# Kernel optimization log

Hardware: AMD Instinct MI355X
Metric: run time of the kernel (lower is better)

Reference implementation:

```python
import jax, jax.numpy as jnp
import numpy as np

N_LVL = [131072, 32768, 8192, 2048, 512, 256]  # active voxels per pyramid level
B = 8          # point clouds in batch
K = 27         # 3x3x3 kernel offsets
SLOPE = 0.01   # LeakyReLU default negative slope
EPS = 1e-5     # BatchNorm eps


def _bn(x, g, b):
    # MinkowskiBatchNorm, training-mode forward: stats over all points
    m = x.mean(0)
    v = x.var(0)
    return (x - m) * jax.lax.rsqrt(v + EPS) * g + b


def _lrelu(x):
    return jnp.where(x >= 0, x, SLOPE * x)


def _lin_block(x, w, g, b):
    # MinkowskiLinear(bias=False) + BN + LeakyReLU (also models 1x1 conv)
    return _lrelu(_bn(x @ w, g, b))


def _conv_block(x, nbr, w, g, b):
    # sparse conv as gather-GEMM: [N,K,Cin] x [K,Cin,Cout] -> [N,Cout]
    y = jnp.einsum('nkc,kco->no', x[nbr], w)
    return _lrelu(_bn(y, g, b))


def _maxpool(x, pmap):
    # stride-2 kernel-3 sparse max pool via precomputed pooling map
    return x[pmap].max(axis=1)


def setup_inputs() -> dict:
    key = jax.random.key(0)
    ks = iter(jax.random.split(key, 80))

    def nrm(shape, scale):
        return jax.random.normal(next(ks), shape, dtype=jnp.float32) * jnp.float32(scale)

    inp = {}
    inp['x'] = nrm((N_LVL[0], 3), 1.0)
    inp['w_mlp1'] = nrm((3, 16), 1.0 / np.sqrt(3.0))
    inp['g_mlp1'] = jnp.ones(16, jnp.float32)
    inp['b_mlp1'] = jnp.zeros(16, jnp.float32)
    conv_dims = [(16, 32), (32, 48), (48, 96), (96, 128), (128, 256), (256, 512)]
    down_dims = [(48, 32), (80, 48), (144, 96), (224, 128), (384, 256)]
    for i, (ci, co) in enumerate(conv_dims):
        inp[f'w_c{i+1}'] = nrm((K, ci, co), np.sqrt(2.0 / (K * co)))  # kaiming fan_out
        inp[f'g_c{i+1}'] = jnp.ones(co, jnp.float32)
        inp[f'b_c{i+1}'] = jnp.zeros(co, jnp.float32)
    for i, (ci, co) in enumerate(down_dims):
        inp[f'w_d{i+1}'] = nrm((ci, co), np.sqrt(2.0 / co))
        inp[f'g_d{i+1}'] = jnp.ones(co, jnp.float32)
        inp[f'b_d{i+1}'] = jnp.zeros(co, jnp.float32)
    inp['w_f1'] = nrm((1024, 512), 1.0 / 32.0)
    inp['g_f1'] = jnp.ones(512, jnp.float32)
    inp['b_f1'] = jnp.zeros(512, jnp.float32)
    inp['w_f2'] = nrm((512, 256), 1.0 / np.sqrt(512.0))
    inp['g_f2'] = jnp.ones(256, jnp.float32)
    inp['b_f2'] = jnp.zeros(256, jnp.float32)
    inp['w_f3'] = nrm((256, 20), 1.0 / 16.0)
    inp['bias_f3'] = jnp.zeros(20, jnp.float32)
    for i in range(6):
        inp[f'nbr{i}'] = jax.random.randint(next(ks), (N_LVL[i], K), 0, N_LVL[i], dtype=jnp.int32)
    for i in range(1, 6):
        inp[f'pool{i}'] = jax.random.randint(next(ks), (N_LVL[i], K), 0, N_LVL[i - 1], dtype=jnp.int32)
    inp['batch5'] = jnp.repeat(jnp.arange(B, dtype=jnp.int32), N_LVL[5] // B)
    return inp


def reference(x, w_mlp1, g_mlp1, b_mlp1,
              w_c1, g_c1, b_c1, w_c2, g_c2, b_c2, w_c3, g_c3, b_c3,
              w_c4, g_c4, b_c4, w_c5, g_c5, b_c5, w_c6, g_c6, b_c6,
              w_d1, g_d1, b_d1, w_d2, g_d2, b_d2, w_d3, g_d3, b_d3,
              w_d4, g_d4, b_d4, w_d5, g_d5, b_d5,
              w_f1, g_f1, b_f1, w_f2, g_f2, b_f2, w_f3, bias_f3,
              nbr0, nbr1, nbr2, nbr3, nbr4, nbr5,
              pool1, pool2, pool3, pool4, pool5, batch5):
    convs = [(w_c1, g_c1, b_c1), (w_c2, g_c2, b_c2), (w_c3, g_c3, b_c3),
             (w_c4, g_c4, b_c4), (w_c5, g_c5, b_c5)]
    downs = [(w_d1, g_d1, b_d1), (w_d2, g_d2, b_d2), (w_d3, g_d3, b_d3),
             (w_d4, g_d4, b_d4), (w_d5, g_d5, b_d5)]
    nbrs = [nbr0, nbr1, nbr2, nbr3, nbr4]
    pools = [pool1, pool2, pool3, pool4, pool5]

    y = _lin_block(x, w_mlp1, g_mlp1, b_mlp1)  # mlp1, level 0
    for i in range(5):  # fixed 5 conv/cat/down/pool stages (structural loop)
        out = _conv_block(y, nbrs[i], *convs[i])
        y = _lin_block(jnp.concatenate([y, out], axis=1), *downs[i])  # cat + down (1x1)
        y = _maxpool(y, pools[i])
    y = _conv_block(y, nbr5, w_c6, g_c6, b_c6)  # conv6 at level 5: [N5, 512]

    xmax = jax.ops.segment_max(y, batch5, num_segments=B)
    cnt = jax.ops.segment_sum(jnp.ones((y.shape[0], 1), y.dtype), batch5, num_segments=B)
    xavg = jax.ops.segment_sum(y, batch5, num_segments=B) / cnt
    z = jnp.concatenate([xmax, xavg], axis=1)  # [B, 1024]

    z = _lin_block(z, w_f1, g_f1, b_f1)  # dropout = identity (eval)
    z = _lin_block(z, w_f2, g_f2, b_f2)
    return z @ w_f3 + bias_f3  # [B, 20] logits
```

## Files before the change

### kernel.cpp

```cpp
#include <hip/hip_runtime.h>
#include <math.h>

#define BN_EPS 1e-5f


__device__ __forceinline__ void fma4(float s, const float4& w, float4& a) {
    a.x = fmaf(s, w.x, a.x);
    a.y = fmaf(s, w.y, a.y);
    a.z = fmaf(s, w.z, a.z);
    a.w = fmaf(s, w.w, a.w);
}

__device__ __forceinline__ float nlr(float x, float sc, float sh) {
    float t = fmaf(x, sc, sh);
    return fmaxf(t, 0.01f * t);
}

__device__ __forceinline__ void bn_coef(const float* __restrict__ sums,
                                        const float* __restrict__ g,
                                        const float* __restrict__ b,
                                        int C, int c, float inv_n,
                                        float& sc, float& sh) {
    float mean = sums[c] * inv_n;
    float var = fmaxf(fmaf(-mean, mean, sums[C + c] * inv_n), 0.f);
    sc = g[c] * rsqrtf(var + BN_EPS);
    sh = fmaf(-mean, sc, b[c]);
}

__global__ void zero_kernel(float* __restrict__ p, int n) {
    int i = blockIdx.x * blockDim.x + threadIdx.x;
    if (i < n) p[i] = 0.f;
}

__global__ void mlp1_kernel(const float* __restrict__ x, const float* __restrict__ w,
                            float* __restrict__ out, int N) {
    int n = blockIdx.x * blockDim.x + threadIdx.x;
    if (n >= N) return;
    float x0 = x[n * 3], x1 = x[n * 3 + 1], x2 = x[n * 3 + 2];
    #pragma unroll
    for (int c4 = 0; c4 < 4; c4++) {
        float4 w0 = *reinterpret_cast<const float4*>(w + 0 + c4 * 4);
        float4 w1 = *reinterpret_cast<const float4*>(w + 16 + c4 * 4);
        float4 w2 = *reinterpret_cast<const float4*>(w + 32 + c4 * 4);
        float4 o;
        o.x = fmaf(x0, w0.x, fmaf(x1, w1.x, x2 * w2.x));
        o.y = fmaf(x0, w0.y, fmaf(x1, w1.y, x2 * w2.y));
        o.z = fmaf(x0, w0.z, fmaf(x1, w1.z, x2 * w2.z));
        o.w = fmaf(x0, w0.w, fmaf(x1, w1.w, x2 * w2.w));
        *reinterpret_cast<float4*>(out + n * 16 + c4 * 4) = o;
    }
}

__global__ void stats4_kernel(const float4* __restrict__ x, int total4, int C, int C4,
                              float* __restrict__ sums) {
    __shared__ float ls[1024];
    int tid = threadIdx.x;
    for (int j = tid; j < 2 * C; j += blockDim.x) ls[j] = 0.f;
    __syncthreads();
    int stride = gridDim.x * blockDim.x;
    int i = blockIdx.x * blockDim.x + tid;
    int c4 = i % C4;
    float4 s = make_float4(0.f, 0.f, 0.f, 0.f);
    float4 q = make_float4(0.f, 0.f, 0.f, 0.f);
    for (; i < total4; i += stride) {
        float4 v = x[i];
        s.x += v.x; s.y += v.y; s.z += v.z; s.w += v.w;
        q.x = fmaf(v.x, v.x, q.x); q.y = fmaf(v.y, v.y, q.y);
        q.z = fmaf(v.z, v.z, q.z); q.w = fmaf(v.w, v.w, q.w);
    }
    int cb = c4 * 4;
    atomicAdd(&ls[cb + 0], s.x); atomicAdd(&ls[cb + 1], s.y);
    atomicAdd(&ls[cb + 2], s.z); atomicAdd(&ls[cb + 3], s.w);
    atomicAdd(&ls[C + cb + 0], q.x); atomicAdd(&ls[C + cb + 1], q.y);
    atomicAdd(&ls[C + cb + 2], q.z); atomicAdd(&ls[C + cb + 3], q.w);
    __syncthreads();
    for (int j = tid; j < 2 * C; j += blockDim.x) atomicAdd(&sums[j], ls[j]);
}

template <int CIN, int COUT, int CO_TILE, int TM, int NTHR, int NQ, int KT,
          bool NORM_IN, bool ATOMIC>
__global__ __launch_bounds__(NTHR) void conv3_kernel(
    const float* __restrict__ y, const int* __restrict__ nbr,
    const float* __restrict__ w, float* __restrict__ out,
    const float* __restrict__ sums, const float* __restrict__ gg,
    const float* __restrict__ bb, float inv_n) {
    constexpr int CQT = CO_TILE / (4 * NQ);
    constexpr int MGRP = NTHR / CQT;
    constexpr int RT = TM / MGRP;
    constexpr int LROW = CIN + 4;
    constexpr int SLOTS = TM * (CIN / 4);
    constexpr int GPT = (SLOTS + NTHR - 1) / NTHR;

    __shared__ __align__(16) float a[2][TM * LROW];
    __shared__ __align__(16) float nsc[CIN], nsh[CIN];

    const int tid = threadIdx.x;
    const int m0 = blockIdx.x * TM;
    const int cobase = blockIdx.y * CO_TILE;
    const int k0 = blockIdx.z * KT;
    const int cq = tid % CQT;
    const int mg = tid / CQT;

    if constexpr (NORM_IN) {
        for (int c = tid; c < CIN; c += NTHR) {
            float sc, sh;
            bn_coef(sums, gg, bb, CIN, c, inv_n, sc, sh);
            nsc[c] = sc;
            nsh[c] = sh;
        }
    }

    int mj[GPT], c4j[GPT];
    bool vj[GPT];
    #pragma unroll
    for (int j = 0; j < GPT; j++) {
        int idx = tid + j * NTHR;
        vj[j] = idx < SLOTS;
        int ii = vj[j] ? idx : 0;
        mj[j] = ii / (CIN / 4);
        c4j[j] = ii % (CIN / 4);
    }

    int nidx[GPT];
    #pragma unroll
    for (int j = 0; j < GPT; j++)
        if (vj[j]) nidx[j] = nbr[(m0 + mj[j]) * 27 + k0];
    float4 gv[GPT];
    #pragma unroll
    for (int j = 0; j < GPT; j++)
        if (vj[j]) gv[j] = *reinterpret_cast<const float4*>(
            y + (size_t)nidx[j] * CIN + c4j[j] * 4);
    if (KT > 1) {
        #pragma unroll
        for (int j = 0; j < GPT; j++)
            if (vj[j]) nidx[j] = nbr[(m0 + mj[j]) * 27 + k0 + 1];
    }
    __syncthreads();
    #pragma unroll
    for (int j = 0; j < GPT; j++) {
        if (!vj[j]) continue;
        float4 v = gv[j];
        if constexpr (NORM_IN) {
            float4 sc = *reinterpret_cast<const float4*>(&nsc[c4j[j] * 4]);
            float4 sh = *reinterpret_cast<const float4*>(&nsh[c4j[j] * 4]);
            v.x = nlr(v.x, sc.x, sh.x); v.y = nlr(v.y, sc.y, sh.y);
            v.z = nlr(v.z, sc.z, sh.z); v.w = nlr(v.w, sc.w, sh.w);
        }
        *reinterpret_cast<float4*>(&a[0][mj[j] * LROW + c4j[j] * 4]) = v;
    }
    __syncthreads();

    float4 acc[RT][NQ];
    #pragma unroll
    for (int r = 0; r < RT; r++)
        #pragma unroll
        for (int q = 0; q < NQ; q++) acc[r][q] = make_float4(0.f, 0.f, 0.f, 0.f);

    for (int kk = 0; kk < KT; kk++) {
        const int cur = kk & 1;
        if (kk + 1 < KT) {
            #pragma unroll
            for (int j = 0; j < GPT; j++)
                if (vj[j]) gv[j] = *reinterpret_cast<const float4*>(
                    y + (size_t)nidx[j] * CIN + c4j[j] * 4);
            if (kk + 2 < KT) {
                #pragma unroll
                for (int j = 0; j < GPT; j++)
                    if (vj[j]) nidx[j] = nbr[(m0 + mj[j]) * 27 + k0 + kk + 2];
            }
        }
        const float* wk = w + (size_t)(k0 + kk) * CIN * COUT + cobase + cq * (4 * NQ);
        const float* ar = &a[cur][mg * LROW];
        #pragma unroll 8
        for (int ci4 = 0; ci4 < CIN / 4; ci4++) {
            float4 wv[4][NQ];
            #pragma unroll
            for (int jj = 0; jj < 4; jj++)
                #pragma unroll
                for (int q = 0; q < NQ; q++)
                    wv[jj][q] = *reinterpret_cast<const float4*>(
                        wk + (size_t)(ci4 * 4 + jj) * COUT + q * 4);
            #pragma unroll
            for (int r = 0; r < RT; r++) {
                float4 av = *reinterpret_cast<const float4*>(&ar[r * MGRP * LROW + ci4 * 4]);
                #pragma unroll
                for (int q = 0; q < NQ; q++) {
                    fma4(av.x, wv[0][q], acc[r][q]);
                    fma4(av.y, wv[1][q], acc[r][q]);
                    fma4(av.z, wv[2][q], acc[r][q]);
                    fma4(av.w, wv[3][q], acc[r][q]);
                }
            }
        }
        if (kk + 1 < KT) {
            #pragma unroll
            for (int j = 0; j < GPT; j++) {
                if (!vj[j]) continue;
                float4 v = gv[j];
                if constexpr (NORM_IN) {
                    float4 sc = *reinterpret_cast<const float4*>(&nsc[c4j[j] * 4]);
                    float4 sh = *reinterpret_cast<const float4*>(&nsh[c4j[j] * 4]);
                    v.x = nlr(v.x, sc.x, sh.x); v.y = nlr(v.y, sc.y, sh.y);
                    v.z = nlr(v.z, sc.z, sh.z); v.w = nlr(v.w, sc.w, sh.w);
                }
                *reinterpret_cast<float4*>(&a[cur ^ 1][mj[j] * LROW + c4j[j] * 4]) = v;
            }
        }
        __syncthreads();
    }

    #pragma unroll
    for (int r = 0; r < RT; r++)
        #pragma unroll
        for (int q = 0; q < NQ; q++) {
            float* op = out + (size_t)(m0 + mg + r * MGRP) * COUT + cobase + (cq * NQ + q) * 4;
            if constexpr (ATOMIC) {
                atomicAdd(op + 0, acc[r][q].x);
                atomicAdd(op + 1, acc[r][q].y);
                atomicAdd(op + 2, acc[r][q].z);
                atomicAdd(op + 3, acc[r][q].w);
            } else {
                *reinterpret_cast<float4*>(op) = acc[r][q];
            }
        }
}

template <int C1, int C2, int COUT, int NQ, int NTHR, bool NORM1>
__global__ __launch_bounds__(NTHR) void down3_kernel(
    const float* __restrict__ in1, const float* __restrict__ in2,
    const float* __restrict__ w, float* __restrict__ out,
    const float* __restrict__ s1, const float* __restrict__ g1,
    const float* __restrict__ b1, float inv1,
    const float* __restrict__ s2, const float* __restrict__ g2,
    const float* __restrict__ b2, float inv2) {
    constexpr int CQT = COUT / (4 * NQ);
    constexpr int PAIRS = NTHR / CQT;
    __shared__ __align__(16) float n1c[C1], n1h[C1], n2c[C2], n2h[C2];

    const int tid = threadIdx.x;
    if constexpr (NORM1) {
        for (int c = tid; c < C1; c += NTHR) {
            float sc, sh;
            bn_coef(s1, g1, b1, C1, c, inv1, sc, sh);
            n1c[c] = sc; n1h[c] = sh;
        }
    }
    for (int c = tid; c < C2; c += NTHR) {
        float sc, sh;
        bn_coef(s2, g2, b2, C2, c, inv2, sc, sh);
        n2c[c] = sc; n2h[c] = sh;
    }
    __syncthreads();

    const int cq = tid % CQT;
    const int pr = tid / CQT;
    const int n0 = (blockIdx.x * PAIRS + pr) * 2;

    float4 acc[2][NQ];
    #pragma unroll
    for (int r = 0; r < 2; r++)
        #pragma unroll
        for (int q = 0; q < NQ; q++) acc[r][q] = make_float4(0.f, 0.f, 0.f, 0.f);

    const float* w1 = w + cq * (4 * NQ);
    #pragma unroll 8
    for (int ci4 = 0; ci4 < C1 / 4; ci4++) {
        float4 a0 = *reinterpret_cast<const float4*>(in1 + (size_t)n0 * C1 + ci4 * 4);
        float4 a1 = *reinterpret_cast<const float4*>(in1 + (size_t)(n0 + 1) * C1 + ci4 * 4);
        if constexpr (NORM1) {
            float4 sc = *reinterpret_cast<const float4*>(&n1c[ci4 * 4]);
            float4 sh = *reinterpret_cast<const float4*>(&n1h[ci4 * 4]);
            a0.x = nlr(a0.x, sc.x, sh.x); a0.y = nlr(a0.y, sc.y, sh.y);
            a0.z = nlr(a0.z, sc.z, sh.z); a0.w = nlr(a0.w, sc.w, sh.w);
            a1.x = nlr(a1.x, sc.x, sh.x); a1.y = nlr(a1.y, sc.y, sh.y);
            a1.z = nlr(a1.z, sc.z, sh.z); a1.w = nlr(a1.w, sc.w, sh.w);
        }
        #pragma unroll
        for (int jj = 0; jj < 4; jj++) {
            const float* wp = w1 + (size_t)(ci4 * 4 + jj) * COUT;
            #pragma unroll
            for (int q = 0; q < NQ; q++) {
                float4 wv = *reinterpret_cast<const float4*>(wp + q * 4);
                float e0 = jj == 0 ? a0.x : jj == 1 ? a0.y : jj == 2 ? a0.z : a0.w;
                float e1 = jj == 0 ? a1.x : jj == 1 ? a1.y : jj == 2 ? a1.z : a1.w;
                fma4(e0, wv, acc[0][q]);
                fma4(e1, wv, acc[1][q]);
            }
        }
    }
    const float* w2 = w + (size_t)C1 * COUT + cq * (4 * NQ);
    #pragma unroll 8
    for (int ci4 = 0; ci4 < C2 / 4; ci4++) {
        float4 a0 = *reinterpret_cast<const float4*>(in2 + (size_t)n0 * C2 + ci4 * 4);
        float4 a1 = *reinterpret_cast<const float4*>(in2 + (size_t)(n0 + 1) * C2 + ci4 * 4);
        float4 sc = *reinterpret_cast<const float4*>(&n2c[ci4 * 4]);
        float4 sh = *reinterpret_cast<const float4*>(&n2h[ci4 * 4]);
        a0.x = nlr(a0.x, sc.x, sh.x); a0.y = nlr(a0.y, sc.y, sh.y);
        a0.z = nlr(a0.z, sc.z, sh.z); a0.w = nlr(a0.w, sc.w, sh.w);
        a1.x = nlr(a1.x, sc.x, sh.x); a1.y = nlr(a1.y, sc.y, sh.y);
        a1.z = nlr(a1.z, sc.z, sh.z); a1.w = nlr(a1.w, sc.w, sh.w);
        #pragma unroll
        for (int jj = 0; jj < 4; jj++) {
            const float* wp = w2 + (size_t)(ci4 * 4 + jj) * COUT;
            #pragma unroll
            for (int q = 0; q < NQ; q++) {
                float4 wv = *reinterpret_cast<const float4*>(wp + q * 4);
                float e0 = jj == 0 ? a0.x : jj == 1 ? a0.y : jj == 2 ? a0.z : a0.w;
                float e1 = jj == 0 ? a1.x : jj == 1 ? a1.y : jj == 2 ? a1.z : a1.w;
                fma4(e0, wv, acc[0][q]);
                fma4(e1, wv, acc[1][q]);
            }
        }
    }
    #pragma unroll
    for (int r = 0; r < 2; r++)
        #pragma unroll
        for (int q = 0; q < NQ; q++)
            *reinterpret_cast<float4*>(out + (size_t)(n0 + r) * COUT + cq * (4 * NQ) + q * 4) =
                acc[r][q];
}

template <int C, int NTHR>
__global__ __launch_bounds__(NTHR) void pool2_kernel(
    const float* __restrict__ draw, const int* __restrict__ pmap,
    const float* __restrict__ sums, const float* __restrict__ g,
    const float* __restrict__ b, float inv_n,
    float* __restrict__ yout, int Nout) {
    constexpr int C4 = C / 4;
    int i = blockIdx.x * NTHR + threadIdx.x;
    if (i >= Nout * C4) return;
    int n = i / C4, c4 = i % C4;
    float sc[4], sh[4];
    #pragma unroll
    for (int j = 0; j < 4; j++) bn_coef(sums, g, b, C, c4 * 4 + j, inv_n, sc[j], sh[j]);
    const int* pm = pmap + n * 27;
    float4 mn = make_float4(INFINITY, INFINITY, INFINITY, INFINITY);
    float4 mx = make_float4(-INFINITY, -INFINITY, -INFINITY, -INFINITY);
    #pragma unroll 9
    for (int k = 0; k < 27; k++) {
        int row = pm[k];
        float4 v = *reinterpret_cast<const float4*>(draw + (size_t)row * C + c4 * 4);
        mn.x = fminf(mn.x, v.x); mn.y = fminf(mn.y, v.y);
        mn.z = fminf(mn.z, v.z); mn.w = fminf(mn.w, v.w);
        mx.x = fmaxf(mx.x, v.x); mx.y = fmaxf(mx.y, v.y);
        mx.z = fmaxf(mx.z, v.z); mx.w = fmaxf(mx.w, v.w);
    }
    float4 o;
    o.x = nlr(sc[0] >= 0.f ? mx.x : mn.x, sc[0], sh[0]);
    o.y = nlr(sc[1] >= 0.f ? mx.y : mn.y, sc[1], sh[1]);
    o.z = nlr(sc[2] >= 0.f ? mx.z : mn.z, sc[2], sh[2]);
    o.w = nlr(sc[3] >= 0.f ? mx.w : mn.w, sc[3], sh[3]);
    *reinterpret_cast<float4*>(yout + (size_t)n * C + c4 * 4) = o;
}

__global__ void segpool2_kernel(const float* __restrict__ y,
                                const float* __restrict__ sums,
                                const float* __restrict__ g, const float* __restrict__ b,
                                float inv_n, float* __restrict__ z) {
    int bi = blockIdx.x;
    int c = threadIdx.x;
    float sc, sh;
    bn_coef(sums, g, b, 512, c, inv_n, sc, sh);
    float mn = INFINITY, mx = -INFINITY, sm = 0.f;
    for (int r = 0; r < 32; r++) {
        float v = y[(size_t)(bi * 32 + r) * 512 + c];
        mn = fminf(mn, v);
        mx = fmaxf(mx, v);
        sm += nlr(v, sc, sh);
    }
    z[bi * 1024 + c] = nlr(sc >= 0.f ? mx : mn, sc, sh);
    z[bi * 1024 + 512 + c] = sm * (1.f / 32.f);
}

template <int K, int COUT, int KSPLIT, bool NORM>
__global__ __launch_bounds__(256) void fc_kernel(
    const float* __restrict__ z, const float* __restrict__ w,
    const float* __restrict__ ns, const float* __restrict__ ng,
    const float* __restrict__ nb, float inv_n,
    float* __restrict__ out) {
    constexpr int KC = K / KSPLIT;
    constexpr int KG = KC / 16;
    __shared__ __align__(16) float zt[KC * 8];
    __shared__ float red[16 * 520];

    const int cobase = blockIdx.x * 64;
    const int kc0 = blockIdx.y * KC;
    const int tid = threadIdx.x;
    const int coq = tid & 15;
    const int kg = tid >> 4;

    for (int idx = tid; idx < 8 * (KC / 4); idx += 256) {
        int n = idx / (KC / 4);
        int kq = idx - n * (KC / 4);
        float4 v = *reinterpret_cast<const float4*>(z + (size_t)n * K + kc0 + kq * 4);
        if constexpr (NORM) {
            #pragma unroll
            for (int j = 0; j < 4; j++) {
                float sc, sh;
                bn_coef(ns, ng, nb, K, kc0 + kq * 4 + j, inv_n, sc, sh);
                float* pv = j == 0 ? &v.x : j == 1 ? &v.y : j == 2 ? &v.z : &v.w;
                *pv = nlr(*pv, sc, sh);
            }
        }
        zt[(kq * 4 + 0) * 8 + n] = v.x;
        zt[(kq * 4 + 1) * 8 + n] = v.y;
        zt[(kq * 4 + 2) * 8 + n] = v.z;
        zt[(kq * 4 + 3) * 8 + n] = v.w;
    }
    __syncthreads();

    float4 acc[8];
    #pragma unroll
    for (int n = 0; n < 8; n++) acc[n] = make_float4(0.f, 0.f, 0.f, 0.f);
    for (int ki = 0; ki < KG; ki++) {
        int k = kg * KG + ki;
        float4 wv = *reinterpret_cast<const float4*>(
            w + (size_t)(kc0 + k) * COUT + cobase + coq * 4);
        float4 za = *reinterpret_cast<const float4*>(&zt[k * 8]);
        float4 zb = *reinterpret_cast<const float4*>(&zt[k * 8 + 4]);
        fma4(za.x, wv, acc[0]); fma4(za.y, wv, acc[1]);
        fma4(za.z, wv, acc[2]); fma4(za.w, wv, acc[3]);
        fma4(zb.x, wv, acc[4]); fma4(zb.y, wv, acc[5]);
        fma4(zb.z, wv, acc[6]); fma4(zb.w, wv, acc[7]);
    }
    #pragma unroll
    for (int n = 0; n < 8; n++) {
        red[kg * 520 + (coq * 4 + 0) * 8 + n] = acc[n].x;
        red[kg * 520 + (coq * 4 + 1) * 8 + n] = acc[n].y;
        red[kg * 520 + (coq * 4 + 2) * 8 + n] = acc[n].z;
        red[kg * 520 + (coq * 4 + 3) * 8 + n] = acc[n].w;
    }
    __syncthreads();
    for (int oi = tid; oi < 512; oi += 256) {
        int c = oi >> 3;
        int n = oi & 7;
        float s = 0.f;
        #pragma unroll
        for (int gg = 0; gg < 16; gg++) s += red[gg * 520 + c * 8 + n];
        float* op = out + (size_t)n * COUT + cobase + c;
        if (KSPLIT > 1) atomicAdd(op, s);
        else *op = s;
    }
}

__global__ void f3n_kernel(const float* __restrict__ in, const float* __restrict__ w,
                           const float* __restrict__ bias,
                           const float* __restrict__ sums, const float* __restrict__ g,
                           const float* __restrict__ b, float inv_n,
                           float* __restrict__ out) {
    __shared__ float zin[8 * 256];
    int tid = threadIdx.x;
    for (int idx = tid; idx < 2048; idx += 256) {
        int c = idx & 255;
        float sc, sh;
        bn_coef(sums, g, b, 256, c, inv_n, sc, sh);
        zin[idx] = nlr(in[idx], sc, sh);
    }
    __syncthreads();
    if (tid >= 160) return;
    int n = tid / 20, co = tid % 20;
    float acc = bias[co];
    for (int ci = 0; ci < 256; ci++)
        acc = fmaf(zin[n * 256 + ci], w[ci * 20 + co], acc);
    out[tid] = acc;
}


extern "C" void kernel_launch(void* const* d_in, const int* in_sizes, int n_in,
                              void* d_out, int out_size, void* d_ws, size_t ws_size,
                              hipStream_t stream) {
    (void)in_sizes; (void)n_in; (void)out_size; (void)ws_size;

    const int N0 = 131072, N1 = 32768, N2 = 8192, N3 = 2048, N4 = 512, N5 = 256;

    const float* x      = (const float*)d_in[0];
    const float* w_mlp1 = (const float*)d_in[1];
    const float* g_mlp1 = (const float*)d_in[2];
    const float* b_mlp1 = (const float*)d_in[3];
    const float* w_c[6]; const float* g_c[6]; const float* b_c[6];
    for (int i = 0; i < 6; i++) {
        w_c[i] = (const float*)d_in[4 + 3 * i];
        g_c[i] = (const float*)d_in[5 + 3 * i];
        b_c[i] = (const float*)d_in[6 + 3 * i];
    }
    const float* w_d[5]; const float* g_d[5]; const float* b_d[5];
    for (int i = 0; i < 5; i++) {
        w_d[i] = (const float*)d_in[22 + 3 * i];
        g_d[i] = (const float*)d_in[23 + 3 * i];
        b_d[i] = (const float*)d_in[24 + 3 * i];
    }
    const float* w_f1 = (const float*)d_in[37];
    const float* g_f1 = (const float*)d_in[38];
    const float* b_f1 = (const float*)d_in[39];
    const float* w_f2 = (const float*)d_in[40];
    const float* g_f2 = (const float*)d_in[41];
    const float* b_f2 = (const float*)d_in[42];
    const float* w_f3 = (const float*)d_in[43];
    const float* bias_f3 = (const float*)d_in[44];
    const int* nbr[6];
    for (int i = 0; i < 6; i++) nbr[i] = (const int*)d_in[45 + i];
    const int* pool[5];
    for (int i = 0; i < 5; i++) pool[i] = (const int*)d_in[51 + i];

    float* ws    = (float*)d_ws;
    float* bufA  = ws;
    float* bufB  = bufA + 2097152;
    float* bufC  = bufB + 4194304;
    float* stats = bufC + 4194304;
    float* out = (float*)d_out;

    auto st = [&](int slot) { return stats + slot * 1024; };
    auto run_stats = [&](const float* buf, int total, int C, int bs, int slot) {
        int total4 = total / 4, C4 = C / 4;
        int gr = (total4 + bs - 1) / bs;
        if (gr > 768) gr = 768;
        stats4_kernel<<<gr, bs, 0, stream>>>((const float4*)buf, total4, C, C4, st(slot));
    };

    const float iN0 = 1.f / N0, iN1 = 1.f / N1, iN2 = 1.f / N2, iN3 = 1.f / N3,
                iN4 = 1.f / N4, iN5 = 1.f / N5, i8 = 1.f / 8.f;

    zero_kernel<<<56, 256, 0, stream>>>(stats, 14 * 1024);

    mlp1_kernel<<<N0 / 256, 256, 0, stream>>>(x, w_mlp1, bufA, N0);
    run_stats(bufA, N0 * 16, 16, 256, 0);

    conv3_kernel<16, 32, 32, 128, 256, 2, 27, true, false>
        <<<dim3(N0 / 128, 1, 1), 256, 0, stream>>>(bufA, nbr[0], w_c[0], bufB,
                                                   st(0), g_mlp1, b_mlp1, iN0);
    run_stats(bufB, N0 * 32, 32, 256, 1);
    down3_kernel<16, 32, 32, 2, 256, true>
        <<<1024, 256, 0, stream>>>(bufA, bufB, w_d[0], bufC,
                                   st(0), g_mlp1, b_mlp1, iN0, st(1), g_c[0], b_c[0], iN0);
    run_stats(bufC, N0 * 32, 32, 256, 2);
    pool2_kernel<32, 256><<<N1 * 8 / 256, 256, 0, stream>>>(
        bufC, pool[0], st(2), g_d[0], b_d[0], iN0, bufA, N1);

    conv3_kernel<32, 48, 48, 64, 192, 2, 27, false, false>
        <<<dim3(N1 / 64, 1, 1), 192, 0, stream>>>(bufA, nbr[1], w_c[1], bufB,
                                                  nullptr, nullptr, nullptr, 0.f);
    run_stats(bufB, N1 * 48, 48, 192, 3);
    down3_kernel<32, 48, 48, 2, 192, false>
        <<<512, 192, 0, stream>>>(bufA, bufB, w_d[1], bufC,
                                  nullptr, nullptr, nullptr, 0.f, st(3), g_c[1], b_c[1], iN1);
    run_stats(bufC, N1 * 48, 48, 192, 4);
    pool2_kernel<48, 192><<<N2 * 12 / 192, 192, 0, stream>>>(
        bufC, pool[1], st(4), g_d[1], b_d[1], iN1, bufA, N2);

    conv3_kernel<48, 96, 48, 64, 192, 2, 27, false, false>
        <<<dim3(N2 / 64, 2, 1), 192, 0, stream>>>(bufA, nbr[2], w_c[2], bufB,
                                                  nullptr, nullptr, nullptr, 0.f);
    run_stats(bufB, N2 * 96, 96, 192, 5);
    down3_kernel<48, 96, 96, 2, 192, false>
        <<<256, 192, 0, stream>>>(bufA, bufB, w_d[2], bufC,
                                  nullptr, nullptr, nullptr, 0.f, st(5), g_c[2], b_c[2], iN2);
    run_stats(bufC, N2 * 96, 96, 192, 6);
    pool2_kernel<96, 192><<<N3 * 24 / 192, 192, 0, stream>>>(
        bufC, pool[2], st(6), g_d[2], b_d[2], iN2, bufA, N3);

    zero_kernel<<<N3 * 128 / 256, 256, 0, stream>>>(bufB, N3 * 128);
    conv3_kernel<96, 128, 64, 64, 256, 2, 9, false, true>
        <<<dim3(N3 / 64, 2, 3), 256, 0, stream>>>(bufA, nbr[3], w_c[3], bufB,
                                                  nullptr, nullptr, nullptr, 0.f);
    run_stats(bufB, N3 * 128, 128, 256, 7);
    down3_kernel<96, 128, 128, 2, 256, false>
        <<<64, 256, 0, stream>>>(bufA, bufB, w_d[3], bufC,
                                 nullptr, nullptr, nullptr, 0.f, st(7), g_c[3], b_c[3], iN3);
    run_stats(bufC, N3 * 128, 128, 256, 8);
    pool2_kernel<128, 256><<<N4 * 32 / 256, 256, 0, stream>>>(
        bufC, pool[3], st(8), g_d[3], b_d[3], iN3, bufA, N4);

    zero_kernel<<<N4 * 256 / 256, 256, 0, stream>>>(bufB, N4 * 256);
    conv3_kernel<128, 256, 64, 32, 128, 2, 3, false, true>
        <<<dim3(N4 / 32, 4, 9), 128, 0, stream>>>(bufA, nbr[4], w_c[4], bufB,
                                                  nullptr, nullptr, nullptr, 0.f);
    run_stats(bufB, N4 * 256, 256, 256, 9);
    down3_kernel<128, 256, 256, 2, 256, false>
        <<<32, 256, 0, stream>>>(bufA, bufB, w_d[4], bufC,
                                 nullptr, nullptr, nullptr, 0.f, st(9), g_c[4], b_c[4], iN4);
    run_stats(bufC, N4 * 256, 256, 256, 10);
    pool2_kernel<256, 256><<<N5 * 64 / 256, 256, 0, stream>>>(
        bufC, pool[4], st(10), g_d[4], b_d[4], iN4, bufA, N5);

    zero_kernel<<<N5 * 512 / 256, 256, 0, stream>>>(bufB, N5 * 512);
    conv3_kernel<256, 512, 64, 16, 128, 1, 3, false, true>
        <<<dim3(N5 / 16, 8, 9), 128, 0, stream>>>(bufA, nbr[5], w_c[5], bufB,
                                                  nullptr, nullptr, nullptr, 0.f);
    run_stats(bufB, N5 * 512, 512, 256, 11);

    segpool2_kernel<<<8, 512, 0, stream>>>(bufB, st(11), g_c[5], b_c[5], iN5, bufC);

    zero_kernel<<<16, 256, 0, stream>>>(bufA, 4096);
    fc_kernel<1024, 512, 4, false><<<dim3(8, 4), 256, 0, stream>>>(
        bufC, w_f1, nullptr, nullptr, nullptr, 0.f, bufA);
    run_stats(bufA, 8 * 512, 512, 256, 12);

    zero_kernel<<<8, 256, 0, stream>>>(bufB, 2048);
    fc_kernel<512, 256, 4, true><<<dim3(4, 4), 256, 0, stream>>>(
        bufA, w_f2, st(12), g_f1, b_f1, i8, bufB);
    run_stats(bufB, 8 * 256, 256, 256, 13);

    f3n_kernel<<<1, 256, 0, stream>>>(bufB, w_f3, bias_f3, st(13), g_f2, b_f2, i8, out);
}
```

Before: 1.184 ms.

## Fuse BN stats into conv/down kernels, replace atomic split-K with partial buffers

Replaces the shared-memory staged gather conv kernel with a direct-gather register-tiled kernel that reads neighbor rows straight from global memory. BatchNorm sum and sum-of-squares are accumulated inside the conv and down kernels, which removes the separate stats passes. The deep levels now write split-K partials to a scratch buffer and reduce them in a kernel that also computes stats, replacing the zero-fill and float atomics. The cost is more global and cache traffic from uncached gathers, plus extra scratch memory for the partials.

```diff
diff --git a/kernel.cpp b/kernel.cpp
--- a/kernel.cpp
+++ b/kernel.cpp
@@ -77,78 +77,83 @@
     for (int j = tid; j < 2 * C; j += blockDim.x) atomicAdd(&sums[j], ls[j]);
 }
 
-template <int CIN, int COUT, int CO_TILE, int TM, int NTHR, int NQ, int KT,
-          bool NORM_IN, bool ATOMIC>
-__global__ __launch_bounds__(NTHR) void conv3_kernel(
+template <int C, int KS>
+__global__ __launch_bounds__(256) void reducek_kernel(
+    const float4* __restrict__ in, float4* __restrict__ out, int total4,
+    float* __restrict__ sums) {
+    __shared__ float ls[1024];
+    constexpr int C4 = C / 4;
+    int tid = threadIdx.x;
+    for (int j = tid; j < 2 * C; j += blockDim.x) ls[j] = 0.f;
+    __syncthreads();
+    int stride = gridDim.x * blockDim.x;
+    int i = blockIdx.x * blockDim.x + tid;
+    int c4 = i % C4;
+    float4 s = make_float4(0.f, 0.f, 0.f, 0.f);
+    float4 q = make_float4(0.f, 0.f, 0.f, 0.f);
+    for (; i < total4; i += stride) {
+        float4 v = make_float4(0.f, 0.f, 0.f, 0.f);
+        #pragma unroll
+        for (int p = 0; p < KS; p++) {
+            float4 t = in[(size_t)p * total4 + i];
+            v.x += t.x; v.y += t.y; v.z += t.z; v.w += t.w;
+        }
+        out[i] = v;
+        s.x += v.x; s.y += v.y; s.z += v.z; s.w += v.w;
+        q.x = fmaf(v.x, v.x, q.x); q.y = fmaf(v.y, v.y, q.y);
+        q.z = fmaf(v.z, v.z, q.z); q.w = fmaf(v.w, v.w, q.w);
+    }
+    int cb = c4 * 4;
+    atomicAdd(&ls[cb + 0], s.x); atomicAdd(&ls[cb + 1], s.y);
+    atomicAdd(&ls[cb + 2], s.z); atomicAdd(&ls[cb + 3], s.w);
+    atomicAdd(&ls[C + cb + 0], q.x); atomicAdd(&ls[C + cb + 1], q.y);
+    atomicAdd(&ls[C + cb + 2], q.z); atomicAdd(&ls[C + cb + 3], q.w);
+    __syncthreads();
+    for (int j = tid; j < 2 * C; j += blockDim.x) atomicAdd(&sums[j], ls[j]);
+}
+
+template <int CIN, int COUT, int CO_TILE, int NCOT, int MT, int TM, int NTHR,
+          int NQ, int KT, bool NORM_IN, bool STATS>
+__global__ __launch_bounds__(NTHR) void convd_kernel(
     const float* __restrict__ y, const int* __restrict__ nbr,
     const float* __restrict__ w, float* __restrict__ out,
-    const float* __restrict__ sums, const float* __restrict__ gg,
-    const float* __restrict__ bb, float inv_n) {
+    const float* __restrict__ s_in, const float* __restrict__ g_in,
+    const float* __restrict__ b_in, float inv_n,
+    float* __restrict__ s_out) {
     constexpr int CQT = CO_TILE / (4 * NQ);
     constexpr int MGRP = NTHR / CQT;
     constexpr int RT = TM / MGRP;
-    constexpr int LROW = CIN + 4;
-    constexpr int SLOTS = TM * (CIN / 4);
-    constexpr int GPT = (SLOTS + NTHR - 1) / NTHR;
-
-    __shared__ __align__(16) float a[2][TM * LROW];
-    __shared__ __align__(16) float nsc[CIN], nsh[CIN];
+    static_assert(MGRP * RT == TM, "tile mismatch");
+
+    __shared__ float nsc[NORM_IN ? CIN : 1];
+    __shared__ float nsh[NORM_IN ? CIN : 1];
+    __shared__ float sred[STATS ? 2 * CO_TILE : 1];
 
     const int tid = threadIdx.x;
-    const int m0 = blockIdx.x * TM;
-    const int cobase = blockIdx.y * CO_TILE;
-    const int k0 = blockIdx.z * KT;
+    const int bid = blockIdx.x;
+    const int cot = bid % NCOT;
+    const int rest = bid / NCOT;
+    const int mt = rest % MT;
+    const int ks = rest / MT;
+    const int m0 = mt * TM;
+    const int cobase = cot * CO_TILE;
+    const int k0 = ks * KT;
     const int cq = tid % CQT;
     const int mg = tid / CQT;
 
     if constexpr (NORM_IN) {
         for (int c = tid; c < CIN; c += NTHR) {
             float sc, sh;
-            bn_coef(sums, gg, bb, CIN, c, inv_n, sc, sh);
+            bn_coef(s_in, g_in, b_in, CIN, c, inv_n, sc, sh);
             nsc[c] = sc;
             nsh[c] = sh;
         }
-    }
-
-    int mj[GPT], c4j[GPT];
-    bool vj[GPT];
-    #pragma unroll
-    for (int j = 0; j < GPT; j++) {
-        int idx = tid + j * NTHR;
-        vj[j] = idx < SLOTS;
-        int ii = vj[j] ? idx : 0;
-        mj[j] = ii / (CIN / 4);
-        c4j[j] = ii % (CIN / 4);
-    }
-
-    int nidx[GPT];
-    #pragma unroll
-    for (int j = 0; j < GPT; j++)
-        if (vj[j]) nidx[j] = nbr[(m0 + mj[j]) * 27 + k0];
-    float4 gv[GPT];
-    #pragma unroll
-    for (int j = 0; j < GPT; j++)
-        if (vj[j]) gv[j] = *reinterpret_cast<const float4*>(
-            y + (size_t)nidx[j] * CIN + c4j[j] * 4);
-    if (KT > 1) {
-        #pragma unroll
-        for (int j = 0; j < GPT; j++)
-            if (vj[j]) nidx[j] = nbr[(m0 + mj[j]) * 27 + k0 + 1];
-    }
-    __syncthreads();
-    #pragma unroll
-    for (int j = 0; j < GPT; j++) {
-        if (!vj[j]) continue;
-        float4 v = gv[j];
-        if constexpr (NORM_IN) {
-            float4 sc = *reinterpret_cast<const float4*>(&nsc[c4j[j] * 4]);
-            float4 sh = *reinterpret_cast<const float4*>(&nsh[c4j[j] * 4]);
-            v.x = nlr(v.x, sc.x, sh.x); v.y = nlr(v.y, sc.y, sh.y);
-            v.z = nlr(v.z, sc.z, sh.z); v.w = nlr(v.w, sc.w, sh.w);
-        }
-        *reinterpret_cast<float4*>(&a[0][mj[j] * LROW + c4j[j] * 4]) = v;
-    }
-    __syncthreads();
+        __syncthreads();
+    }
+
+    int mrow[RT];
+    #pragma unroll
+    for (int r = 0; r < RT; r++) mrow[r] = m0 + mg + r * MGRP;
 
     float4 acc[RT][NQ];
     #pragma unroll
@@ -156,73 +161,83 @@
         #pragma unroll
         for (int q = 0; q < NQ; q++) acc[r][q] = make_float4(0.f, 0.f, 0.f, 0.f);
 
-    for (int kk = 0; kk < KT; kk++) {
-        const int cur = kk & 1;
-        if (kk + 1 < KT) {
+    for (int kk = k0; kk < k0 + KT; kk++) {
+        int rows[RT];
+        #pragma unroll
+        for (int r = 0; r < RT; r++) rows[r] = nbr[(size_t)mrow[r] * 27 + kk];
+        const float* wk = w + (size_t)kk * CIN * COUT + cobase + cq * (4 * NQ);
+        #pragma unroll 4
+        for (int ci4 = 0; ci4 < CIN / 4; ci4++) {
+            float4 yv[RT];
             #pragma unroll
-            for (int j = 0; j < GPT; j++)
-                if (vj[j]) gv[j] = *reinterpret_cast<const float4*>(
-                    y + (size_t)nidx[j] * CIN + c4j[j] * 4);
-            if (kk + 2 < KT) {
+            for (int r = 0; r < RT; r++)
+                yv[r] = *reinterpret_cast<const float4*>(
+                    y + (size_t)rows[r] * CIN + ci4 * 4);
+            if constexpr (NORM_IN) {
+                float4 sc = *reinterpret_cast<const float4*>(&nsc[ci4 * 4]);
+                float4 sh = *reinterpret_cast<const float4*>(&nsh[ci4 * 4]);
                 #pragma unroll
-                for (int j = 0; j < GPT; j++)
-                    if (vj[j]) nidx[j] = nbr[(m0 + mj[j]) * 27 + k0 + kk + 2];
+                for (int r = 0; r < RT; r++) {
+                    yv[r].x = nlr(yv[r].x, sc.x, sh.x);
+                    yv[r].y = nlr(yv[r].y, sc.y, sh.y);
+                    yv[r].z = nlr(yv[r].z, sc.z, sh.z);
+                    yv[r].w = nlr(yv[r].w, sc.w, sh.w);
+                }
             }
-        }
-        const float* wk = w + (size_t)(k0 + kk) * CIN * COUT + cobase + cq * (4 * NQ);
-        const float* ar = &a[cur][mg * LROW];
-        #pragma unroll 8
-        for (int ci4 = 0; ci4 < CIN / 4; ci4++) {
-            float4 wv[4][NQ];
             #pragma unroll
-            for (int jj = 0; jj < 4; jj++)
+            for (int jj = 0; jj < 4; jj++) {
                 #pragma unroll
-                for (int q = 0; q < NQ; q++)
-                    wv[jj][q] = *reinterpret_cast<const float4*>(
+                for (int q = 0; q < NQ; q++) {
+                    float4 wv = *reinterpret_cast<const float4*>(
                         wk + (size_t)(ci4 * 4 + jj) * COUT + q * 4);
+                    #pragma unroll
+                    for (int r = 0; r < RT; r++) {
+                        float e = jj == 0 ? yv[r].x : jj == 1 ? yv[r].y
+                                 : jj == 2 ? yv[r].z : yv[r].w;
+                        fma4(e, wv, acc[r][q]);
+                    }
+                }
+            }
+        }
+    }
+
+    float* outp = out + (size_t)ks * MT * TM * COUT;
+    #pragma unroll
+    for (int r = 0; r < RT; r++)
+        #pragma unroll
+        for (int q = 0; q < NQ; q++)
+            *reinterpret_cast<float4*>(
+                outp + (size_t)mrow[r] * COUT + cobase + cq * (4 * NQ) + q * 4) =
+                acc[r][q];
+
+    if constexpr (STATS) {
+        for (int j = tid; j < 2 * CO_TILE; j += NTHR) sred[j] = 0.f;
+        __syncthreads();
+        #pragma unroll
+        for (int q = 0; q < NQ; q++) {
+            float4 s = make_float4(0.f, 0.f, 0.f, 0.f);
+            float4 qq = make_float4(0.f, 0.f, 0.f, 0.f);
             #pragma unroll
             for (int r = 0; r < RT; r++) {
-                float4 av = *reinterpret_cast<const float4*>(&ar[r * MGRP * LROW + ci4 * 4]);
-                #pragma unroll
-                for (int q = 0; q < NQ; q++) {
-                    fma4(av.x, wv[0][q], acc[r][q]);
-                    fma4(av.y, wv[1][q], acc[r][q]);
-                    fma4(av.z, wv[2][q], acc[r][q]);
-                    fma4(av.w, wv[3][q], acc[r][q]);
-                }
+                float4 v = acc[r][q];
+                s.x += v.x; s.y += v.y; s.z += v.z; s.w += v.w;
+                qq.x = fmaf(v.x, v.x, qq.x); qq.y = fmaf(v.y, v.y, qq.y);
+                qq.z = fmaf(v.z, v.z, qq.z); qq.w = fmaf(v.w, v.w, qq.w);
             }
-        }
-        if (kk + 1 < KT) {
-            #pragma unroll
-            for (int j = 0; j < GPT; j++) {
-                if (!vj[j]) continue;
-                float4 v = gv[j];
-                if constexpr (NORM_IN) {
-                    float4 sc = *reinterpret_cast<const float4*>(&nsc[c4j[j] * 4]);
-                    float4 sh = *reinterpret_cast<const float4*>(&nsh[c4j[j] * 4]);
-                    v.x = nlr(v.x, sc.x, sh.x); v.y = nlr(v.y, sc.y, sh.y);
-                    v.z = nlr(v.z, sc.z, sh.z); v.w = nlr(v.w, sc.w, sh.w);
-                }
-                *reinterpret_cast<float4*>(&a[cur ^ 1][mj[j] * LROW + c4j[j] * 4]) = v;
-            }
+            int cb = cq * (4 * NQ) + q * 4;
+            atomicAdd(&sred[cb + 0], s.x); atomicAdd(&sred[cb + 1], s.y);
+            atomicAdd(&sred[cb + 2], s.z); atomicAdd(&sred[cb + 3], s.w);
+            atomicAdd(&sred[CO_TILE + cb + 0], qq.x);
+            atomicAdd(&sred[CO_TILE + cb + 1], qq.y);
+            atomicAdd(&sred[CO_TILE + cb + 2], qq.z);
+            atomicAdd(&sred[CO_TILE + cb + 3], qq.w);
         }
         __syncthreads();
-    }
-
-    #pragma unroll
-    for (int r = 0; r < RT; r++)
-        #pragma unroll
-        for (int q = 0; q < NQ; q++) {
-            float* op = out + (size_t)(m0 + mg + r * MGRP) * COUT + cobase + (cq * NQ + q) * 4;
-            if constexpr (ATOMIC) {
-                atomicAdd(op + 0, acc[r][q].x);
-                atomicAdd(op + 1, acc[r][q].y);
-                atomicAdd(op + 2, acc[r][q].z);
-                atomicAdd(op + 3, acc[r][q].w);
-            } else {
-                *reinterpret_cast<float4*>(op) = acc[r][q];
-            }
-        }
+        for (int j = tid; j < CO_TILE; j += NTHR) {
+            atomicAdd(&s_out[cobase + j], sred[j]);
+            atomicAdd(&s_out[COUT + cobase + j], sred[CO_TILE + j]);
+        }
+    }
 }
 
 template <int C1, int C2, int COUT, int NQ, int NTHR, bool NORM1>
@@ -232,10 +247,12 @@
     const float* __restrict__ s1, const float* __restrict__ g1,
     const float* __restrict__ b1, float inv1,
     const float* __restrict__ s2, const float* __restrict__ g2,
-    const float* __restrict__ b2, float inv2) {
+    const float* __restrict__ b2, float inv2,
+    float* __restrict__ s_out) {
     constexpr int CQT = COUT / (4 * NQ);
     constexpr int PAIRS = NTHR / CQT;
     __shared__ __align__(16) float n1c[C1], n1h[C1], n2c[C2], n2h[C2];
+    __shared__ float sred[2 * COUT];
 
     const int tid = threadIdx.x;
     if constexpr (NORM1) {
@@ -250,6 +267,7 @@
         bn_coef(s2, g2, b2, C2, c, inv2, sc, sh);
         n2c[c] = sc; n2h[c] = sh;
     }
+    for (int j = tid; j < 2 * COUT; j += NTHR) sred[j] = 0.f;
     __syncthreads();
 
     const int cq = tid % CQT;
@@ -278,11 +296,11 @@
         #pragma unroll
         for (int jj = 0; jj < 4; jj++) {
             const float* wp = w1 + (size_t)(ci4 * 4 + jj) * COUT;
+            float e0 = jj == 0 ? a0.x : jj == 1 ? a0.y : jj == 2 ? a0.z : a0.w;
+            float e1 = jj == 0 ? a1.x : jj == 1 ? a1.y : jj == 2 ? a1.z : a1.w;
             #pragma unroll
             for (int q = 0; q < NQ; q++) {
                 float4 wv = *reinterpret_cast<const float4*>(wp + q * 4);
-                float e0 = jj == 0 ? a0.x : jj == 1 ? a0.y : jj == 2 ? a0.z : a0.w;
-                float e1 = jj == 0 ? a1.x : jj == 1 ? a1.y : jj == 2 ? a1.z : a1.w;
                 fma4(e0, wv, acc[0][q]);
                 fma4(e1, wv, acc[1][q]);
             }
@@ -302,11 +320,11 @@
         #pragma unroll
         for (int jj = 0; jj < 4; jj++) {
             const float* wp = w2 + (size_t)(ci4 * 4 + jj) * COUT;
+            float e0 = jj == 0 ? a0.x : jj == 1 ? a0.y : jj == 2 ? a0.z : a0.w;
+            float e1 = jj == 0 ? a1.x : jj == 1 ? a1.y : jj == 2 ? a1.z : a1.w;
             #pragma unroll
             for (int q = 0; q < NQ; q++) {
                 float4 wv = *reinterpret_cast<const float4*>(wp + q * 4);
-                float e0 = jj == 0 ? a0.x : jj == 1 ? a0.y : jj == 2 ? a0.z : a0.w;
-                float e1 = jj == 0 ? a1.x : jj == 1 ? a1.y : jj == 2 ? a1.z : a1.w;
                 fma4(e0, wv, acc[0][q]);
                 fma4(e1, wv, acc[1][q]);
             }
@@ -318,6 +336,31 @@
         for (int q = 0; q < NQ; q++)
             *reinterpret_cast<float4*>(out + (size_t)(n0 + r) * COUT + cq * (4 * NQ) + q * 4) =
                 acc[r][q];
+
+    #pragma unroll
+    for (int q = 0; q < NQ; q++) {
+        float4 s = make_float4(0.f, 0.f, 0.f, 0.f);
+        float4 qq = make_float4(0.f, 0.f, 0.f, 0.f);
+        #pragma unroll
+        for (int r = 0; r < 2; r++) {
+            float4 v = acc[r][q];
+            s.x += v.x; s.y += v.y; s.z += v.z; s.w += v.w;
+            qq.x = fmaf(v.x, v.x, qq.x); qq.y = fmaf(v.y, v.y, qq.y);
+            qq.z = fmaf(v.z, v.z, qq.z); qq.w = fmaf(v.w, v.w, qq.w);
+        }
+        int cb = cq * (4 * NQ) + q * 4;
+        atomicAdd(&sred[cb + 0], s.x); atomicAdd(&sred[cb + 1], s.y);
+        atomicAdd(&sred[cb + 2], s.z); atomicAdd(&sred[cb + 3], s.w);
+        atomicAdd(&sred[COUT + cb + 0], qq.x);
+        atomicAdd(&sred[COUT + cb + 1], qq.y);
+        atomicAdd(&sred[COUT + cb + 2], qq.z);
+        atomicAdd(&sred[COUT + cb + 3], qq.w);
+    }
+    __syncthreads();
+    for (int j = tid; j < COUT; j += NTHR) {
+        atomicAdd(&s_out[j], sred[j]);
+        atomicAdd(&s_out[COUT + j], sred[COUT + j]);
+    }
 }
 
 template <int C, int NTHR>
@@ -525,68 +568,65 @@
     mlp1_kernel<<<N0 / 256, 256, 0, stream>>>(x, w_mlp1, bufA, N0);
     run_stats(bufA, N0 * 16, 16, 256, 0);
 
-    conv3_kernel<16, 32, 32, 128, 256, 2, 27, true, false>
-        <<<dim3(N0 / 128, 1, 1), 256, 0, stream>>>(bufA, nbr[0], w_c[0], bufB,
-                                                   st(0), g_mlp1, b_mlp1, iN0);
-    run_stats(bufB, N0 * 32, 32, 256, 1);
+    convd_kernel<16, 32, 32, 1, 1024, 128, 256, 2, 27, true, true>
+        <<<1024, 256, 0, stream>>>(bufA, nbr[0], w_c[0], bufB,
+                                   st(0), g_mlp1, b_mlp1, iN0, st(1));
     down3_kernel<16, 32, 32, 2, 256, true>
         <<<1024, 256, 0, stream>>>(bufA, bufB, w_d[0], bufC,
-                                   st(0), g_mlp1, b_mlp1, iN0, st(1), g_c[0], b_c[0], iN0);
-    run_stats(bufC, N0 * 32, 32, 256, 2);
+                                   st(0), g_mlp1, b_mlp1, iN0,
+                                   st(1), g_c[0], b_c[0], iN0, st(2));
     pool2_kernel<32, 256><<<N1 * 8 / 256, 256, 0, stream>>>(
         bufC, pool[0], st(2), g_d[0], b_d[0], iN0, bufA, N1);
 
-    conv3_kernel<32, 48, 48, 64, 192, 2, 27, false, false>
-        <<<dim3(N1 / 64, 1, 1), 192, 0, stream>>>(bufA, nbr[1], w_c[1], bufB,
-                                                  nullptr, nullptr, nullptr, 0.f);
-    run_stats(bufB, N1 * 48, 48, 192, 3);
+    convd_kernel<32, 48, 48, 1, 512, 64, 192, 2, 27, false, true>
+        <<<512, 192, 0, stream>>>(bufA, nbr[1], w_c[1], bufB,
+                                  nullptr, nullptr, nullptr, 0.f, st(3));
     down3_kernel<32, 48, 48, 2, 192, false>
         <<<512, 192, 0, stream>>>(bufA, bufB, w_d[1], bufC,
-                                  nullptr, nullptr, nullptr, 0.f, st(3), g_c[1], b_c[1], iN1);
-    run_stats(bufC, N1 * 48, 48, 192, 4);
+                                  nullptr, nullptr, nullptr, 0.f,
+                                  st(3), g_c[1], b_c[1], iN1, st(4));
     pool2_kernel<48, 192><<<N2 * 12 / 192, 192, 0, stream>>>(
         bufC, pool[1], st(4), g_d[1], b_d[1], iN1, bufA, N2);
 
-    conv3_kernel<48, 96, 48, 64, 192, 2, 27, false, false>
-        <<<dim3(N2 / 64, 2, 1), 192, 0, stream>>>(bufA, nbr[2], w_c[2], bufB,
-                                                  nullptr, nullptr, nullptr, 0.f);
-    run_stats(bufB, N2 * 96, 96, 192, 5);
+    convd_kernel<48, 96, 48, 2, 128, 64, 192, 2, 27, false, true>
+        <<<256, 192, 0, stream>>>(bufA, nbr[2], w_c[2], bufB,
+                                  nullptr, nullptr, nullptr, 0.f, st(5));
     down3_kernel<48, 96, 96, 2, 192, false>
         <<<256, 192, 0, stream>>>(bufA, bufB, w_d[2], bufC,
-                                  nullptr, nullptr, nullptr, 0.f, st(5), g_c[2], b_c[2], iN2);
-    run_stats(bufC, N2 * 96, 96, 192, 6);
+                                  nullptr, nullptr, nullptr, 0.f,
+                                  st(5), g_c[2], b_c[2], iN2, st(6));
     pool2_kernel<96, 192><<<N3 * 24 / 192, 192, 0, stream>>>(
         bufC, pool[2], st(6), g_d[2], b_d[2], iN2, bufA, N3);
 
-    zero_kernel<<<N3 * 128 / 256, 256, 0, stream>>>(bufB, N3 * 128);
-    conv3_kernel<96, 128, 64, 64, 256, 2, 9, false, true>
-        <<<dim3(N3 / 64, 2, 3), 256, 0, stream>>>(bufA, nbr[3], w_c[3], bufB,
-                                                  nullptr, nullptr, nullptr, 0.f);
-    run_stats(bufB, N3 * 128, 128, 256, 7);
+    convd_kernel<96, 128, 64, 2, 32, 64, 256, 2, 3, false, false>
+        <<<576, 256, 0, stream>>>(bufA, nbr[3], w_c[3], bufC,
+                                  nullptr, nullptr, nullptr, 0.f, nullptr);
+    reducek_kernel<128, 9><<<256, 256, 0, stream>>>(
+        (const float4*)bufC, (float4*)bufB, N3 * 32, st(7));
     down3_kernel<96, 128, 128, 2, 256, false>
         <<<64, 256, 0, stream>>>(bufA, bufB, w_d[3], bufC,
-                                 nullptr, nullptr, nullptr, 0.f, st(7), g_c[3], b_c[3], iN3);
-    run_stats(bufC, N3 * 128, 128, 256, 8);
+                                 nullptr, nullptr, nullptr, 0.f,
+                                 st(7), g_c[3], b_c[3], iN3, st(8));
     pool2_kernel<128, 256><<<N4 * 32 / 256, 256, 0, stream>>>(
         bufC, pool[3], st(8), g_d[3], b_d[3], iN3, bufA, N4);
 
-    zero_kernel<<<N4 * 256 / 256, 256, 0, stream>>>(bufB, N4 * 256);
-    conv3_kernel<128, 256, 64, 32, 128, 2, 3, false, true>
-        <<<dim3(N4 / 32, 4, 9), 128, 0, stream>>>(bufA, nbr[4], w_c[4], bufB,
-                                                  nullptr, nullptr, nullptr, 0.f);
-    run_stats(bufB, N4 * 256, 256, 256, 9);
+    convd_kernel<128, 256, 64, 4, 8, 64, 256, 2, 3, false, false>
+        <<<288, 256, 0, stream>>>(bufA, nbr[4], w_c[4], bufC,
+                                  nullptr, nullptr, nullptr, 0.f, nullptr);
+    reducek_kernel<256, 9><<<128, 256, 0, stream>>>(
+        (const float4*)bufC, (float4*)bufB, N4 * 64, st(9));
     down3_kernel<128, 256, 256, 2, 256, false>
         <<<32, 256, 0, stream>>>(bufA, bufB, w_d[4], bufC,
-                                 nullptr, nullptr, nullptr, 0.f, st(9), g_c[4], b_c[4], iN4);
-    run_stats(bufC, N4 * 256, 256, 256, 10);
+                                 nullptr, nullptr, nullptr, 0.f,
+                                 st(9), g_c[4], b_c[4], iN4, st(10));
     pool2_kernel<256, 256><<<N5 * 64 / 256, 256, 0, stream>>>(
         bufC, pool[4], st(10), g_d[4], b_d[4], iN4, bufA, N5);
 
-    zero_kernel<<<N5 * 512 / 256, 256, 0, stream>>>(bufB, N5 * 512);
-    conv3_kernel<256, 512, 64, 16, 128, 1, 3, false, true>
-        <<<dim3(N5 / 16, 8, 9), 128, 0, stream>>>(bufA, nbr[5], w_c[5], bufB,
-                                                  nullptr, nullptr, nullptr, 0.f);
-    run_stats(bufB, N5 * 512, 512, 256, 11);
+    convd_kernel<256, 512, 64, 8, 4, 64, 256, 2, 1, false, false>
+        <<<864, 256, 0, stream>>>(bufA, nbr[5], w_c[5], bufC,
+                                  nullptr, nullptr, nullptr, 0.f, nullptr);
+    reducek_kernel<512, 27><<<128, 256, 0, stream>>>(
+        (const float4*)bufC, (float4*)bufB, N5 * 128, st(11));
 
     segpool2_kernel<<<8, 512, 0, stream>>>(bufB, st(11), g_c[5], b_c[5], iN5, bufC);
 
```

New measurement: 1.148 ms. -3.0%, faster.
